# Kernel tuning notes

Measured on AMD Instinct MI355X. Metric: run time of the kernel, lower is better.

## Reference

```python
import jax, jax.numpy as jnp
import numpy as np

B, T, F, H, O = 4096, 64, 89, 1024, 89


def setup_inputs() -> dict:
    key = jax.random.key(0)
    k1, k2, k3, k4 = jax.random.split(key, 4)
    x = jax.random.normal(k1, (B, T, F), dtype=jnp.float32)
    # Keras LSTM params: kernel [F,4H], recurrent_kernel [H,4H], bias [4H]; gate order i,f,c,o
    Wk = jax.random.normal(k2, (F, 4 * H), dtype=jnp.float32) * 0.05
    Wr = jax.random.normal(k3, (H, 4 * H), dtype=jnp.float32) * 0.05
    b = jnp.zeros((4 * H,), dtype=jnp.float32)
    Wd = jax.random.normal(k4, (H, O), dtype=jnp.float32) * 0.05
    bd = jnp.zeros((O,), dtype=jnp.float32)
    return {"x": x, "Wk": Wk, "Wr": Wr, "b": b, "Wd": Wd, "bd": bd}


def _lstm_relu(x, Wk, Wr, b):
    # activation='relu' (cell candidate & cell output), recurrent_activation=sigmoid
    hidden = Wr.shape[0]
    xz = jnp.einsum('btf,fg->btg', x, Wk) + b  # precompute input projection [B,T,4H]

    def step(carry, xz_t):
        h, c = carry
        z = xz_t + h @ Wr  # [B,4H]
        i, f, g, o = jnp.split(z, 4, axis=-1)
        i = jax.nn.sigmoid(i)
        f = jax.nn.sigmoid(f)
        g = jax.nn.relu(g)
        o = jax.nn.sigmoid(o)
        c = f * c + i * g
        h = o * jax.nn.relu(c)
        return (h, c), None

    h0 = jnp.zeros((x.shape[0], hidden), dtype=x.dtype)
    c0 = jnp.zeros_like(h0)
    (h_last, _), _ = jax.lax.scan(step, (h0, c0), jnp.swapaxes(xz, 0, 1))
    return h_last


def reference(x, Wk, Wr, b, Wd, bd):
    h_last = _lstm_relu(x, Wk, Wr, b)  # only last timestep is used by dense
    return h_last @ Wd + bd
```

## Files before the change

### kernel.cpp

```cpp
#include <hip/hip_runtime.h>
#include <hip/hip_bf16.h>

#define B_SZ 4096
#define T_SZ 64
#define F_SZ 89
#define H_SZ 1024
#define O_SZ 89
#define KX   128
#define KTOT (KX + H_SZ)
#define NSL  (KTOT / 32)

typedef __attribute__((ext_vector_type(8))) short bf16x8;
typedef __attribute__((ext_vector_type(4))) float f32x4;

__device__ __forceinline__ void gload_lds16(const void* g, void* l) {
  __builtin_amdgcn_global_load_lds((const __attribute__((address_space(1))) void*)g,
                                   (__attribute__((address_space(3))) void*)l,
                                   16, 0, 0);
}
__device__ __forceinline__ float sigmoidf_(float x) {
  return 1.0f / (1.0f + __expf(-x));
}

__global__ __launch_bounds__(256) void pack_w(const float* __restrict__ Wk,
                                              const float* __restrict__ Wr,
                                              __hip_bfloat16* __restrict__ WT2) {
  __shared__ float tile[64][65];
  const int n0 = blockIdx.x * 64;
  const int k0 = blockIdx.y * 64;
  const int c  = threadIdx.x & 63;
  const int rq = threadIdx.x >> 6;
  for (int j = 0; j < 16; ++j) {
    int kk = rq * 16 + j;
    int k = k0 + kk;
    float v;
    if (k < KX) v = (k < F_SZ) ? Wk[(size_t)k * 4096 + n0 + c] : 0.0f;
    else        v = Wr[(size_t)(k - KX) * 4096 + n0 + c];
    tile[kk][c] = v;
  }
  __syncthreads();
  for (int j = 0; j < 16; ++j) {
    int R = n0 + rq * 16 + j;
    int g = R >> 10, h = R & 1023;
    int np = ((h >> 4) << 6) + (g << 4) + (h & 15);
    WT2[(size_t)np * KTOT + k0 + c] = __float2bfloat16(tile[c][rq * 16 + j]);
  }
}

__global__ __launch_bounds__(256) void pack_x(const float* __restrict__ x,
                                              __hip_bfloat16* __restrict__ xp) {
  const int wid = (blockIdx.x * 256 + threadIdx.x) >> 6;
  const int l   = threadIdx.x & 63;
  for (int r = wid; r < T_SZ * B_SZ; r += 8192) {
    const int t = r >> 12, m = r & 4095;
    const float* src = x + ((size_t)m * T_SZ + t) * F_SZ;
    float v0 = src[l];
    float v1 = (64 + l < F_SZ) ? src[64 + l] : 0.0f;
    __hip_bfloat16* dst = xp + (size_t)r * KX;
    dst[l]      = __float2bfloat16(v0);
    dst[64 + l] = __float2bfloat16(v1);
  }
}

__global__ __launch_bounds__(256) void pack_wd(const float* __restrict__ Wd,
                                               __hip_bfloat16* __restrict__ WdT2) {
  int o = blockIdx.x;
  for (int k = threadIdx.x; k < 1024; k += 256) {
    float v = (o < O_SZ) ? Wd[(size_t)k * O_SZ + o] : 0.0f;
    __hip_bfloat16 w1 = __float2bfloat16(v);
    WdT2[(size_t)o * 1024 + k] = w1;
    WdT2[96 * 1024 + (size_t)o * 1024 + k] = __float2bfloat16(v - __bfloat162float(w1));
  }
}

__global__ __launch_bounds__(512, 2)
void lstm_step(const __hip_bfloat16* __restrict__ xp_t,
               const __hip_bfloat16* __restrict__ h_in,
               __hip_bfloat16* __restrict__ h_out,
               float* __restrict__ cbuf,
               const __hip_bfloat16* __restrict__ WT2,
               const float* __restrict__ bias,
               __hip_bfloat16* __restrict__ h2_out)
{
  __shared__ __attribute__((aligned(1024))) char smem[131072];

  const int tid  = threadIdx.x;
  const int lane = tid & 63;
  const int w    = tid >> 6;
  const int wm   = w >> 2;
  const int wn   = w & 3;

  const int bid = blockIdx.x;
  const int wg  = (bid & 7) * 32 + (bid >> 3);
  const int bx  = wg >> 4;
  const int by  = wg & 15;
  const int m0  = bx * 256;

  const int s_rl = lane >> 2;
  const int s_cb = (((lane & 3) ^ ((lane >> 3) & 3)) << 4);
  const int lr = lane & 15, lq = lane >> 4;
  const int cc = ((lq ^ ((lr >> 1) & 3)) << 4);

  const char* bsrc0 = (const char*)(WT2 + (size_t)by * 256 * KTOT);

  f32x4 acc[8][4];
#pragma unroll
  for (int mi = 0; mi < 8; ++mi)
#pragma unroll
    for (int ni = 0; ni < 4; ++ni) acc[mi][ni] = (f32x4){0.f, 0.f, 0.f, 0.f};

  auto stageA = [&](int s) {
    const char* base; int ldb;
    if (s < 4) { base = (const char*)xp_t + ((size_t)m0 * KX) * 2 + s * 64;           ldb = KX * 2; }
    else       { base = (const char*)h_in + ((size_t)m0 * H_SZ) * 2 + (s * 64 - 256); ldb = H_SZ * 2; }
    char* slot = smem + (s & 3) * 16384;
#pragma unroll
    for (int j = 0; j < 2; ++j) {
      int row = (j * 8 + w) * 16 + s_rl;
      gload_lds16(base + (size_t)row * ldb + s_cb, slot + (j * 8 + w) * 1024);
    }
  };
  auto stageB = [&](int s) {
    char* slot = smem + 65536 + (s & 3) * 16384;
#pragma unroll
    for (int j = 0; j < 2; ++j) {
      int row = (j * 8 + w) * 16 + s_rl;
      gload_lds16(bsrc0 + (size_t)row * (KTOT * 2) + s * 64 + s_cb, slot + (j * 8 + w) * 1024);
    }
  };

  stageA(0); stageB(0);
  stageA(1); stageB(1);
  asm volatile("s_waitcnt vmcnt(4)" ::: "memory");
  __builtin_amdgcn_s_barrier();

  for (int ks = 0; ks < NSL; ++ks) {
    const char* Aslot = smem + (ks & 3) * 16384;
    const char* Bslot = smem + 65536 + (ks & 3) * 16384;

    bf16x8 Bf[4], Af[8];
#pragma unroll
    for (int ni = 0; ni < 4; ++ni)
      Bf[ni] = *(const bf16x8*)(Bslot + (wn * 64 + ni * 16 + lr) * 64 + cc);
#pragma unroll
    for (int mi = 0; mi < 8; ++mi)
      Af[mi] = *(const bf16x8*)(Aslot + (wm * 128 + mi * 16 + lr) * 64 + cc);

    if (ks < NSL - 2) { stageA(ks + 2); stageB(ks + 2); }

    __builtin_amdgcn_s_setprio(1);
#pragma unroll
    for (int mi = 0; mi < 8; ++mi)
#pragma unroll
      for (int ni = 0; ni < 4; ++ni)
        acc[mi][ni] = __builtin_amdgcn_mfma_f32_16x16x32_bf16(Af[mi], Bf[ni], acc[mi][ni], 0, 0, 0);
    __builtin_amdgcn_s_setprio(0);

    if (ks < NSL - 2)       asm volatile("s_waitcnt vmcnt(4)" ::: "memory");
    else if (ks == NSL - 2) asm volatile("s_waitcnt vmcnt(0)" ::: "memory");
    if (ks < NSL - 1) __builtin_amdgcn_s_barrier();
  }

  const int hcol = by * 64 + wn * 16 + lr;
  const float b0 = bias[hcol];
  const float b1 = bias[H_SZ + hcol];
  const float b2 = bias[2 * H_SZ + hcol];
  const float b3 = bias[3 * H_SZ + hcol];
#pragma unroll
  for (int mi = 0; mi < 8; ++mi) {
#pragma unroll
    for (int v = 0; v < 4; ++v) {
      int r = m0 + wm * 128 + mi * 16 + lq * 4 + v;
      size_t idx = (size_t)r * H_SZ + hcol;
      float iv = sigmoidf_(acc[mi][0][v] + b0);
      float fv = sigmoidf_(acc[mi][1][v] + b1);
      float gv = fmaxf(acc[mi][2][v] + b2, 0.0f);
      float ov = sigmoidf_(acc[mi][3][v] + b3);
      float cn = fv * cbuf[idx] + iv * gv;
      cbuf[idx] = cn;
      float hv = ov * fmaxf(cn, 0.0f);
      __hip_bfloat16 h1 = __float2bfloat16(hv);
      h_out[idx] = h1;
      if (h2_out) h2_out[idx] = __float2bfloat16(hv - __bfloat162float(h1));
    }
  }
}

__global__ __launch_bounds__(256)
void dense_k(const __hip_bfloat16* __restrict__ h1,
             const __hip_bfloat16* __restrict__ h2,
             const __hip_bfloat16* __restrict__ WdT2,
             const float* __restrict__ bd,
             float* __restrict__ out) {
  __shared__ __attribute__((aligned(1024))) char smem[8192 + 12288];
  const int tid = threadIdx.x, lane = tid & 63, w = tid >> 6;
  const int m0 = blockIdx.x * 64;
  const int lr = lane & 15, lq = lane >> 4;
  const int s_cb = (((lane & 7) ^ ((lane >> 3) & 7)) << 4);

  f32x4 acc[6];
#pragma unroll
  for (int ni = 0; ni < 6; ++ni) acc[ni] = (f32x4){0.f, 0.f, 0.f, 0.f};

  for (int p = 0; p < 3; ++p) {
    const __hip_bfloat16* Asrc = (p < 2) ? h1 : h2;
    const __hip_bfloat16* Bsrc = WdT2 + (p == 1 ? 96 * 1024 : 0);
    for (int kb = 0; kb < 16; ++kb) {
      __syncthreads();
#pragma unroll
      for (int j = 0; j < 2; ++j) {
        int row = j * 32 + w * 8 + (lane >> 3);
        gload_lds16((const char*)(Asrc + (size_t)(m0 + row) * 1024 + kb * 64) + s_cb,
                    smem + j * 4096 + w * 1024);
      }
#pragma unroll
      for (int j = 0; j < 3; ++j) {
        int row = j * 32 + w * 8 + (lane >> 3);
        gload_lds16((const char*)(Bsrc + (size_t)row * 1024 + kb * 64) + s_cb,
                    smem + 8192 + j * 4096 + w * 1024);
      }
      __syncthreads();

      bf16x8 Af[2], Bf[6][2];
#pragma unroll
      for (int ks = 0; ks < 2; ++ks)
        Af[ks] = *(const bf16x8*)(smem + (w * 16 + lr) * 128 + (((4 * ks + lq) ^ (lr & 7)) << 4));
#pragma unroll
      for (int ni = 0; ni < 6; ++ni)
#pragma unroll
        for (int ks = 0; ks < 2; ++ks)
          Bf[ni][ks] = *(const bf16x8*)(smem + 8192 + (ni * 16 + lr) * 128 + (((4 * ks + lq) ^ (lr & 7)) << 4));
#pragma unroll
      for (int ni = 0; ni < 6; ++ni)
#pragma unroll
        for (int ks = 0; ks < 2; ++ks)
          acc[ni] = __builtin_amdgcn_mfma_f32_16x16x32_bf16(Af[ks], Bf[ni][ks], acc[ni], 0, 0, 0);
    }
  }

#pragma unroll
  for (int ni = 0; ni < 6; ++ni) {
    int o = ni * 16 + lr;
    if (o < O_SZ) {
      float bv = bd[o];
#pragma unroll
      for (int v = 0; v < 4; ++v) {
        int r = m0 + w * 16 + lq * 4 + v;
        out[(size_t)r * O_SZ + o] = acc[ni][v] + bv;
      }
    }
  }
}

extern "C" void kernel_launch(void* const* d_in, const int* in_sizes, int n_in,
                              void* d_out, int out_size, void* d_ws, size_t ws_size,
                              hipStream_t stream) {
  const float* x  = (const float*)d_in[0];
  const float* Wk = (const float*)d_in[1];
  const float* Wr = (const float*)d_in[2];
  const float* b  = (const float*)d_in[3];
  const float* Wd = (const float*)d_in[4];
  const float* bd = (const float*)d_in[5];
  float* out = (float*)d_out;

  char* ws = (char*)d_ws;
  size_t off = 0;
  auto carve = [&](size_t bytes) -> char* {
    char* p = ws + off;
    off += (bytes + 255) & ~(size_t)255;
    return p;
  };
  __hip_bfloat16* WT2  = (__hip_bfloat16*)carve((size_t)4096 * KTOT * 2);
  __hip_bfloat16* xp   = (__hip_bfloat16*)carve((size_t)T_SZ * B_SZ * KX * 2);
  __hip_bfloat16* h0   = (__hip_bfloat16*)carve((size_t)B_SZ * H_SZ * 2);
  __hip_bfloat16* h1b  = (__hip_bfloat16*)carve((size_t)B_SZ * H_SZ * 2);
  float*          cbuf = (float*)carve((size_t)B_SZ * H_SZ * 4);
  __hip_bfloat16* h2   = (__hip_bfloat16*)carve((size_t)B_SZ * H_SZ * 2);
  __hip_bfloat16* WdT2 = (__hip_bfloat16*)carve((size_t)2 * 96 * 1024 * 2);

  hipMemsetAsync(h0, 0, (size_t)B_SZ * H_SZ * 2, stream);
  hipMemsetAsync(cbuf, 0, (size_t)B_SZ * H_SZ * 4, stream);

  pack_w<<<dim3(64, 18), 256, 0, stream>>>(Wk, Wr, WT2);
  pack_x<<<2048, 256, 0, stream>>>(x, xp);
  pack_wd<<<96, 256, 0, stream>>>(Wd, WdT2);

  __hip_bfloat16* hbuf[2] = {h0, h1b};
  for (int t = 0; t < T_SZ; ++t) {
    const __hip_bfloat16* xpt = xp + (size_t)t * B_SZ * KX;
    lstm_step<<<256, 512, 0, stream>>>(xpt, hbuf[t & 1], hbuf[(t + 1) & 1], cbuf, WT2, b,
                                       (t == T_SZ - 1) ? h2 : nullptr);
  }

  dense_k<<<64, 256, 0, stream>>>(hbuf[0], h2, WdT2, bd, out);
}
```

Measured before the change: 2.964 ms.

## Deepen LSTM GEMM pipeline with register double-buffered fragments and specialize first step

Reworks the per-step GEMM main loop to prefetch three K-slices into LDS and to double-buffer the MFMA operand fragments in registers. LDS reads for the next slice are interleaved between the two halves of the MFMA work, which hides LDS latency behind matrix ops. The first timestep gets its own template instantiation: since h and c start at zero, it runs only the 4 x-slices and skips the forget gate and the cell-state read. The memsets are dropped in exchange. This costs more registers, which could hurt the 2-blocks-per-CU occupancy target.

```diff
diff --git a/kernel.cpp b/kernel.cpp
--- a/kernel.cpp
+++ b/kernel.cpp
@@ -8,7 +8,7 @@
 #define O_SZ 89
 #define KX   128
 #define KTOT (KX + H_SZ)
-#define NSL  (KTOT / 32)
+#define NSL_FULL (KTOT / 32)
 
 typedef __attribute__((ext_vector_type(8))) short bf16x8;
 typedef __attribute__((ext_vector_type(4))) float f32x4;
@@ -51,6 +51,7 @@
                                               __hip_bfloat16* __restrict__ xp) {
   const int wid = (blockIdx.x * 256 + threadIdx.x) >> 6;
   const int l   = threadIdx.x & 63;
+#pragma unroll 4
   for (int r = wid; r < T_SZ * B_SZ; r += 8192) {
     const int t = r >> 12, m = r & 4095;
     const float* src = x + ((size_t)m * T_SZ + t) * F_SZ;
@@ -73,6 +74,7 @@
   }
 }
 
+template <int NSL, bool FIRST>
 __global__ __launch_bounds__(512, 2)
 void lstm_step(const __hip_bfloat16* __restrict__ xp_t,
                const __hip_bfloat16* __restrict__ h_in,
@@ -100,6 +102,8 @@
   const int s_cb = (((lane & 3) ^ ((lane >> 3) & 3)) << 4);
   const int lr = lane & 15, lq = lane >> 4;
   const int cc = ((lq ^ ((lr >> 1) & 3)) << 4);
+  const int aoff = (wm * 128 + lr) * 64 + cc;
+  const int boff = (wn * 64 + lr) * 64 + cc;
 
   const char* bsrc0 = (const char*)(WT2 + (size_t)by * 256 * KTOT);
 
@@ -129,43 +133,74 @@
     }
   };
 
-  stageA(0); stageB(0);
-  stageA(1); stageB(1);
-  asm volatile("s_waitcnt vmcnt(4)" ::: "memory");
-  __builtin_amdgcn_s_barrier();
-
-  for (int ks = 0; ks < NSL; ++ks) {
-    const char* Aslot = smem + (ks & 3) * 16384;
-    const char* Bslot = smem + 65536 + (ks & 3) * 16384;
-
-    bf16x8 Bf[4], Af[8];
-#pragma unroll
-    for (int ni = 0; ni < 4; ++ni)
-      Bf[ni] = *(const bf16x8*)(Bslot + (wn * 64 + ni * 16 + lr) * 64 + cc);
-#pragma unroll
-    for (int mi = 0; mi < 8; ++mi)
-      Af[mi] = *(const bf16x8*)(Aslot + (wm * 128 + mi * 16 + lr) * 64 + cc);
-
-    if (ks < NSL - 2) { stageA(ks + 2); stageB(ks + 2); }
-
+  bf16x8 AfA[8], BfA[4], AfB[8], BfB[4];
+
+  auto frag_read0 = [&](int s, bf16x8 (&Af)[8], bf16x8 (&Bf)[4]) {
+    const char* An = smem + (s & 3) * 16384;
+    const char* Bn = smem + 65536 + (s & 3) * 16384;
+#pragma unroll
+    for (int ni = 0; ni < 4; ++ni) Bf[ni] = *(const bf16x8*)(Bn + boff + ni * 1024);
+#pragma unroll
+    for (int mi = 0; mi < 4; ++mi) Af[mi] = *(const bf16x8*)(An + aoff + mi * 1024);
+  };
+  auto frag_read1 = [&](int s, bf16x8 (&Af)[8]) {
+    const char* An = smem + (s & 3) * 16384;
+#pragma unroll
+    for (int mi = 4; mi < 8; ++mi) Af[mi] = *(const bf16x8*)(An + aoff + mi * 1024);
+  };
+  auto mfma_h0 = [&](bf16x8 (&Af)[8], bf16x8 (&Bf)[4]) {
     __builtin_amdgcn_s_setprio(1);
 #pragma unroll
-    for (int mi = 0; mi < 8; ++mi)
+    for (int mi = 0; mi < 4; ++mi)
 #pragma unroll
       for (int ni = 0; ni < 4; ++ni)
         acc[mi][ni] = __builtin_amdgcn_mfma_f32_16x16x32_bf16(Af[mi], Bf[ni], acc[mi][ni], 0, 0, 0);
     __builtin_amdgcn_s_setprio(0);
-
-    if (ks < NSL - 2)       asm volatile("s_waitcnt vmcnt(4)" ::: "memory");
-    else if (ks == NSL - 2) asm volatile("s_waitcnt vmcnt(0)" ::: "memory");
-    if (ks < NSL - 1) __builtin_amdgcn_s_barrier();
+  };
+  auto mfma_h1 = [&](bf16x8 (&Af)[8], bf16x8 (&Bf)[4]) {
+    __builtin_amdgcn_s_setprio(1);
+#pragma unroll
+    for (int mi = 4; mi < 8; ++mi)
+#pragma unroll
+      for (int ni = 0; ni < 4; ++ni)
+        acc[mi][ni] = __builtin_amdgcn_mfma_f32_16x16x32_bf16(Af[mi], Bf[ni], acc[mi][ni], 0, 0, 0);
+    __builtin_amdgcn_s_setprio(0);
+  };
+
+  auto body = [&](int ks, bf16x8 (&ACur)[8], bf16x8 (&BCur)[4],
+                  bf16x8 (&ANxt)[8], bf16x8 (&BNxt)[4]) {
+    if (ks + 3 < NSL) { stageA(ks + 3); stageB(ks + 3); }
+    mfma_h0(ACur, BCur);
+    if (ks + 1 < NSL) frag_read0(ks + 1, ANxt, BNxt);
+    mfma_h1(ACur, BCur);
+    if (ks + 1 < NSL) frag_read1(ks + 1, ANxt);
+    if (ks + 3 < NSL)       asm volatile("s_waitcnt vmcnt(4)" ::: "memory");
+    else if (ks + 3 == NSL) asm volatile("s_waitcnt vmcnt(0)" ::: "memory");
+    if (ks + 1 < NSL) __builtin_amdgcn_s_barrier();
+  };
+
+  stageA(0); stageB(0);
+  stageA(1); stageB(1);
+  stageA(2); stageB(2);
+  asm volatile("s_waitcnt vmcnt(8)" ::: "memory");
+  __builtin_amdgcn_s_barrier();
+  frag_read0(0, AfA, BfA);
+  frag_read1(0, AfA);
+  asm volatile("s_waitcnt vmcnt(4)" ::: "memory");
+  __builtin_amdgcn_s_barrier();
+
+#pragma unroll 1
+  for (int kp = 0; kp < NSL / 2; ++kp) {
+    body(2 * kp,     AfA, BfA, AfB, BfB);
+    body(2 * kp + 1, AfB, BfB, AfA, BfA);
   }
 
   const int hcol = by * 64 + wn * 16 + lr;
   const float b0 = bias[hcol];
-  const float b1 = bias[H_SZ + hcol];
   const float b2 = bias[2 * H_SZ + hcol];
   const float b3 = bias[3 * H_SZ + hcol];
+  float b1 = 0.0f;
+  if constexpr (!FIRST) b1 = bias[H_SZ + hcol];
 #pragma unroll
   for (int mi = 0; mi < 8; ++mi) {
 #pragma unroll
@@ -173,10 +208,15 @@
       int r = m0 + wm * 128 + mi * 16 + lq * 4 + v;
       size_t idx = (size_t)r * H_SZ + hcol;
       float iv = sigmoidf_(acc[mi][0][v] + b0);
-      float fv = sigmoidf_(acc[mi][1][v] + b1);
       float gv = fmaxf(acc[mi][2][v] + b2, 0.0f);
       float ov = sigmoidf_(acc[mi][3][v] + b3);
-      float cn = fv * cbuf[idx] + iv * gv;
+      float cn;
+      if constexpr (FIRST) {
+        cn = iv * gv;
+      } else {
+        float fv = sigmoidf_(acc[mi][1][v] + b1);
+        cn = fv * cbuf[idx] + iv * gv;
+      }
       cbuf[idx] = cn;
       float hv = ov * fmaxf(cn, 0.0f);
       __hip_bfloat16 h1 = __float2bfloat16(hv);
@@ -278,18 +318,17 @@
   __hip_bfloat16* h2   = (__hip_bfloat16*)carve((size_t)B_SZ * H_SZ * 2);
   __hip_bfloat16* WdT2 = (__hip_bfloat16*)carve((size_t)2 * 96 * 1024 * 2);
 
-  hipMemsetAsync(h0, 0, (size_t)B_SZ * H_SZ * 2, stream);
-  hipMemsetAsync(cbuf, 0, (size_t)B_SZ * H_SZ * 4, stream);
-
   pack_w<<<dim3(64, 18), 256, 0, stream>>>(Wk, Wr, WT2);
   pack_x<<<2048, 256, 0, stream>>>(x, xp);
   pack_wd<<<96, 256, 0, stream>>>(Wd, WdT2);
 
   __hip_bfloat16* hbuf[2] = {h0, h1b};
-  for (int t = 0; t < T_SZ; ++t) {
+  lstm_step<4, true><<<256, 512, 0, stream>>>(xp, hbuf[0], hbuf[1], cbuf, WT2, b, nullptr);
+  for (int t = 1; t < T_SZ; ++t) {
     const __hip_bfloat16* xpt = xp + (size_t)t * B_SZ * KX;
-    lstm_step<<<256, 512, 0, stream>>>(xpt, hbuf[t & 1], hbuf[(t + 1) & 1], cbuf, WT2, b,
-                                       (t == T_SZ - 1) ? h2 : nullptr);
+    lstm_step<NSL_FULL, false><<<256, 512, 0, stream>>>(xpt, hbuf[t & 1], hbuf[(t + 1) & 1],
+                                                        cbuf, WT2, b,
+                                                        (t == T_SZ - 1) ? h2 : nullptr);
   }
 
   dense_k<<<64, 256, 0, stream>>>(hbuf[0], h2, WdT2, bd, out);
```

Measured after the change: 2.982 ms. No clear change (+0.6%).
